# Optimization experiments

Measured on AMD Instinct MI355X. Metric: run time of the kernel, lower is better.

The kernel has to match this reference:

```python
import jax, jax.numpy as jnp
import numpy as np

B, C, H, W = 2, 1, 2048, 2048
RADIUS = 1
RK = 2 * RADIUS + 1  # 3
N = H * W
OBV_DECAY = 0.95


def setup_inputs() -> dict:
    key = jax.random.key(0)
    k1, k2, k3, k4, k5 = jax.random.split(key, 5)
    # x: [B, C+1, H, W]; channel 0 = spin field s, last channel = inverse temperature b (>0)
    x = jax.random.uniform(k1, (B, C + 1, H, W), dtype=jnp.float32)
    obvs = jax.random.uniform(k2, (B, 4, H, W), dtype=jnp.float32)
    # learned coupling table, center tap zeroed (no self-coupling)
    J = jax.random.uniform(k3, (1, RK * RK, N), dtype=jnp.float32)
    J = J.at[:, RADIUS * RK + RADIUS, :].set(0.0)
    # explicit RNG draws (torch.rand_like equivalents) for determinism
    rand_s = jax.random.uniform(k4, (B, C, H, W), dtype=jnp.float32)
    rand_drop = jax.random.uniform(k5, (1, 1, H, W), dtype=jnp.float32)
    return {"x": x, "obvs": obvs, "J": J, "rand_s": rand_s, "rand_drop": rand_drop}


def _unfold3(s):
    # F.unfold(circular_pad(s,1), 3) for a single-channel map: [B,1,H,W] -> [B,9,H*W]
    sp = jnp.pad(s, ((0, 0), (0, 0), (1, 1), (1, 1)), mode='wrap')
    patches = jnp.stack(
        [sp[:, 0, i:i + H, j:j + W] for i in range(RK) for j in range(RK)], axis=1
    )  # [B, 9, H, W], kernel positions row-major (matches F.unfold)
    return patches.reshape(s.shape[0], RK * RK, N)


def reference(x, obvs, J, rand_s, rand_drop):
    s = x[:, :C]          # [B,1,H,W] spins
    b = x[:, -1:]         # [B,1,H,W] inverse temperature
    sf = s.reshape(s.shape[0], 1, N)                 # unfold(s, 1)
    sJs = 2.0 * sf * (_unfold3(s) * J)               # [B,9,N]
    delta_e = sJs.sum(axis=1).reshape(s.shape)       # [B,1,H,W]
    E = -0.5 * delta_e

    # EMA observables
    e, e2, c, m = obvs[:, 0:1], obvs[:, 1:2], obvs[:, 2:3], obvs[:, 3:4]
    d = OBV_DECAY
    e = d * e + (1.0 - d) * E
    e2 = d * e2 + (1.0 - d) * E ** 2
    c = d * c + (1.0 - d) * (e2 - e ** 2) * b ** 2
    m = d * m + (1.0 - d) * s
    obvs_out = jnp.concatenate([e, e2, c, m], axis=1)  # [B,4,H,W]

    p = jnp.where(delta_e <= 0.0, jnp.ones_like(s), jnp.exp(-delta_e * b))
    accept = (rand_s < p) & (rand_drop > 0.5)
    flip = -2.0 * accept.astype(s.dtype) + 1.0

    state = jnp.concatenate([s * flip, b], axis=1)    # [B,2,H,W]
    return state, obvs_out
```

## Files before the change

kernel.cpp:

```cpp
#include <hip/hip_runtime.h>
#include <math.h>

namespace {
constexpr int H = 2048;
constexpr int W = 2048;
constexpr int NPIX = H * W;
constexpr int B = 2;
constexpr float DECf = 0.95f;
constexpr float OMDf = 1.0f - 0.95f;
}

using f4 = __attribute__((ext_vector_type(4))) float;

__global__ __launch_bounds__(256, 4) void ising_step_kernel(
    const float* __restrict__ x,
    const float* __restrict__ obvs,
    const float* __restrict__ Jm,
    const float* __restrict__ rs,
    const float* __restrict__ rd,
    float* __restrict__ out)
{
  const int bid = blockIdx.x;
  const int u   = ((bid & 7) << 10) | (bid >> 3);
  const int bi  = u >> 12;
  const int h   = (u >> 1) & (H - 1);
  const int w0  = ((u & 1) << 10) | (threadIdx.x << 2);
  const int n0  = (h << 11) | w0;

  const float* sbase = x + (size_t)bi * 2 * NPIX;
  const int hm = (h - 1) & (H - 1);
  const int hp = (h + 1) & (H - 1);
  const float* rowm = sbase + (size_t)hm * W;
  const float* rowc = sbase + (size_t)h  * W;
  const float* rowp = sbase + (size_t)hp * W;
  const int wl = (w0 - 1) & (W - 1);
  const int wr = (w0 + 4) & (W - 1);

  const f4 vm = *(const f4*)(rowm + w0);
  const f4 vc = *(const f4*)(rowc + w0);
  const f4 vp = *(const f4*)(rowp + w0);
  const float lm = rowm[wl], rm = rowm[wr];
  const float lc = rowc[wl], rc = rowc[wr];
  const float lp = rowp[wl], rp = rowp[wr];

  f4 jv[8];
  #pragma unroll
  for (int k = 0; k < 8; ++k) {
    const int kk = (k < 4) ? k : (k + 1);
    jv[k] = *(const f4*)(Jm + (size_t)kk * NPIX + n0);
  }

  const f4 bv  = *(const f4*)(sbase + (size_t)NPIX + n0);
  const float* ob = obvs + (size_t)bi * 4 * NPIX + n0;
  const f4 ev  = *(const f4*)(ob);
  const f4 e2v = *(const f4*)(ob + (size_t)NPIX);
  const f4 cv  = *(const f4*)(ob + 2 * (size_t)NPIX);
  const f4 mv  = *(const f4*)(ob + 3 * (size_t)NPIX);
  const f4 rv  = *(const f4*)(rs + (size_t)bi * NPIX + n0);
  const f4 dv  = *(const f4*)(rd + n0);

  const float am[6] = {lm, vm.x, vm.y, vm.z, vm.w, rm};
  const float ac[6] = {lc, vc.x, vc.y, vc.z, vc.w, rc};
  const float ap[6] = {lp, vp.x, vp.y, vp.z, vp.w, rp};

  const float bq[4]  = {bv.x, bv.y, bv.z, bv.w};
  const float eq[4]  = {ev.x, ev.y, ev.z, ev.w};
  const float e2q[4] = {e2v.x, e2v.y, e2v.z, e2v.w};
  const float cq[4]  = {cv.x, cv.y, cv.z, cv.w};
  const float mq[4]  = {mv.x, mv.y, mv.z, mv.w};
  const float rsq[4] = {rv.x, rv.y, rv.z, rv.w};
  const float rdq[4] = {dv.x, dv.y, dv.z, dv.w};

  float so[4], eo[4], e2o[4], co[4], mo[4];
  #pragma unroll
  for (int t = 0; t < 4; ++t) {
    const double sum =
        (double)jv[0][t] * am[t]     + (double)jv[1][t] * am[t + 1] +
        (double)jv[2][t] * am[t + 2] + (double)jv[3][t] * ac[t]     +
        (double)jv[4][t] * ac[t + 2] + (double)jv[5][t] * ap[t]     +
        (double)jv[6][t] * ap[t + 1] + (double)jv[7][t] * ap[t + 2];
    const float sf  = ac[t + 1];
    const double s  = (double)sf;
    const double de = 2.0 * s * sum;
    const double p  = (de <= 0.0) ? 1.0 : exp(-de * (double)bq[t]);
    const bool acc  = ((double)rsq[t] < p) && (rdq[t] > 0.5f);
    const float E   = (float)(-s * sum);
    const float bf  = bq[t];
    const float en  = DECf * eq[t]  + OMDf * E;
    const float e2n = DECf * e2q[t] + OMDf * E * E;
    const float cn  = DECf * cq[t]  + OMDf * (e2n - en * en) * bf * bf;
    const float mn  = DECf * mq[t]  + OMDf * sf;
    so[t]  = acc ? -sf : sf;
    eo[t]  = en;
    e2o[t] = e2n;
    co[t]  = cn;
    mo[t]  = mn;
  }

  float* st = out + (size_t)bi * 2 * NPIX;
  float* oo = out + (size_t)B * 2 * NPIX + (size_t)bi * 4 * NPIX;
  *(f4*)(st + n0)                     = (f4){so[0], so[1], so[2], so[3]};
  *(f4*)(st + (size_t)NPIX + n0)      = bv;
  *(f4*)(oo + n0)                     = (f4){eo[0], eo[1], eo[2], eo[3]};
  *(f4*)(oo + (size_t)NPIX + n0)      = (f4){e2o[0], e2o[1], e2o[2], e2o[3]};
  *(f4*)(oo + 2 * (size_t)NPIX + n0)  = (f4){co[0], co[1], co[2], co[3]};
  *(f4*)(oo + 3 * (size_t)NPIX + n0)  = (f4){mo[0], mo[1], mo[2], mo[3]};
}

extern "C" void kernel_launch(void* const* d_in, const int* in_sizes, int n_in,
                              void* d_out, int out_size, void* d_ws, size_t ws_size,
                              hipStream_t stream) {
  const float* x    = (const float*)d_in[0];
  const float* obvs = (const float*)d_in[1];
  const float* Jm   = (const float*)d_in[2];
  const float* rs   = (const float*)d_in[3];
  const float* rd   = (const float*)d_in[4];
  float* out = (float*)d_out;

  constexpr int grid = B * H * 2;
  ising_step_kernel<<<grid, 256, 0, stream>>>(x, obvs, Jm, rs, rd, out);
}
```

Baseline: 123.1 us.

## Process both batch elements per thread to reuse coupling and dropout loads

Each thread now computes both batch elements for its pixels, so the shared J coupling table and dropout mask are loaded once instead of once per batch. The grid is halved accordingly, the block-index swizzle is adjusted, and the occupancy hint is removed from launch bounds. This cuts global memory traffic for a bandwidth-bound kernel. In exchange it raises register pressure and per-thread latency exposure.

```diff
diff --git a/kernel.cpp b/kernel.cpp
--- a/kernel.cpp
+++ b/kernel.cpp
@@ -12,7 +12,7 @@
 
 using f4 = __attribute__((ext_vector_type(4))) float;
 
-__global__ __launch_bounds__(256, 4) void ising_step_kernel(
+__global__ __launch_bounds__(256) void ising_step_kernel(
     const float* __restrict__ x,
     const float* __restrict__ obvs,
     const float* __restrict__ Jm,
@@ -21,27 +21,15 @@
     float* __restrict__ out)
 {
   const int bid = blockIdx.x;
-  const int u   = ((bid & 7) << 10) | (bid >> 3);
-  const int bi  = u >> 12;
-  const int h   = (u >> 1) & (H - 1);
+  const int u   = ((bid & 7) << 9) | (bid >> 3);
+  const int h   = u >> 1;
   const int w0  = ((u & 1) << 10) | (threadIdx.x << 2);
   const int n0  = (h << 11) | w0;
 
-  const float* sbase = x + (size_t)bi * 2 * NPIX;
   const int hm = (h - 1) & (H - 1);
   const int hp = (h + 1) & (H - 1);
-  const float* rowm = sbase + (size_t)hm * W;
-  const float* rowc = sbase + (size_t)h  * W;
-  const float* rowp = sbase + (size_t)hp * W;
   const int wl = (w0 - 1) & (W - 1);
   const int wr = (w0 + 4) & (W - 1);
-
-  const f4 vm = *(const f4*)(rowm + w0);
-  const f4 vc = *(const f4*)(rowc + w0);
-  const f4 vp = *(const f4*)(rowp + w0);
-  const float lm = rowm[wl], rm = rowm[wr];
-  const float lc = rowc[wl], rc = rowc[wr];
-  const float lp = rowp[wl], rp = rowp[wr];
 
   f4 jv[8];
   #pragma unroll
@@ -49,62 +37,79 @@
     const int kk = (k < 4) ? k : (k + 1);
     jv[k] = *(const f4*)(Jm + (size_t)kk * NPIX + n0);
   }
+  const f4 dv = *(const f4*)(rd + n0);
 
-  const f4 bv  = *(const f4*)(sbase + (size_t)NPIX + n0);
-  const float* ob = obvs + (size_t)bi * 4 * NPIX + n0;
-  const f4 ev  = *(const f4*)(ob);
-  const f4 e2v = *(const f4*)(ob + (size_t)NPIX);
-  const f4 cv  = *(const f4*)(ob + 2 * (size_t)NPIX);
-  const f4 mv  = *(const f4*)(ob + 3 * (size_t)NPIX);
-  const f4 rv  = *(const f4*)(rs + (size_t)bi * NPIX + n0);
-  const f4 dv  = *(const f4*)(rd + n0);
-
-  const float am[6] = {lm, vm.x, vm.y, vm.z, vm.w, rm};
-  const float ac[6] = {lc, vc.x, vc.y, vc.z, vc.w, rc};
-  const float ap[6] = {lp, vp.x, vp.y, vp.z, vp.w, rp};
-
-  const float bq[4]  = {bv.x, bv.y, bv.z, bv.w};
-  const float eq[4]  = {ev.x, ev.y, ev.z, ev.w};
-  const float e2q[4] = {e2v.x, e2v.y, e2v.z, e2v.w};
-  const float cq[4]  = {cv.x, cv.y, cv.z, cv.w};
-  const float mq[4]  = {mv.x, mv.y, mv.z, mv.w};
-  const float rsq[4] = {rv.x, rv.y, rv.z, rv.w};
-  const float rdq[4] = {dv.x, dv.y, dv.z, dv.w};
-
-  float so[4], eo[4], e2o[4], co[4], mo[4];
+  f4 vm[2], vc[2], vp[2], bv[2], ev[2], e2v[2], cv[2], mv[2], rv[2];
+  float lm[2], rmh[2], lc[2], rch[2], lp[2], rph[2];
   #pragma unroll
-  for (int t = 0; t < 4; ++t) {
-    const double sum =
-        (double)jv[0][t] * am[t]     + (double)jv[1][t] * am[t + 1] +
-        (double)jv[2][t] * am[t + 2] + (double)jv[3][t] * ac[t]     +
-        (double)jv[4][t] * ac[t + 2] + (double)jv[5][t] * ap[t]     +
-        (double)jv[6][t] * ap[t + 1] + (double)jv[7][t] * ap[t + 2];
-    const float sf  = ac[t + 1];
-    const double s  = (double)sf;
-    const double de = 2.0 * s * sum;
-    const double p  = (de <= 0.0) ? 1.0 : exp(-de * (double)bq[t]);
-    const bool acc  = ((double)rsq[t] < p) && (rdq[t] > 0.5f);
-    const float E   = (float)(-s * sum);
-    const float bf  = bq[t];
-    const float en  = DECf * eq[t]  + OMDf * E;
-    const float e2n = DECf * e2q[t] + OMDf * E * E;
-    const float cn  = DECf * cq[t]  + OMDf * (e2n - en * en) * bf * bf;
-    const float mn  = DECf * mq[t]  + OMDf * sf;
-    so[t]  = acc ? -sf : sf;
-    eo[t]  = en;
-    e2o[t] = e2n;
-    co[t]  = cn;
-    mo[t]  = mn;
+  for (int bi = 0; bi < 2; ++bi) {
+    const float* sb   = x + (size_t)bi * 2 * NPIX;
+    const float* rowm = sb + (size_t)hm * W;
+    const float* rowc = sb + (size_t)h  * W;
+    const float* rowp = sb + (size_t)hp * W;
+    vm[bi] = *(const f4*)(rowm + w0);
+    vc[bi] = *(const f4*)(rowc + w0);
+    vp[bi] = *(const f4*)(rowp + w0);
+    lm[bi] = rowm[wl];  rmh[bi] = rowm[wr];
+    lc[bi] = rowc[wl];  rch[bi] = rowc[wr];
+    lp[bi] = rowp[wl];  rph[bi] = rowp[wr];
+    bv[bi] = *(const f4*)(sb + (size_t)NPIX + n0);
+    const float* ob = obvs + (size_t)bi * 4 * NPIX + n0;
+    ev[bi]  = *(const f4*)(ob);
+    e2v[bi] = *(const f4*)(ob + (size_t)NPIX);
+    cv[bi]  = *(const f4*)(ob + 2 * (size_t)NPIX);
+    mv[bi]  = *(const f4*)(ob + 3 * (size_t)NPIX);
+    rv[bi]  = *(const f4*)(rs + (size_t)bi * NPIX + n0);
   }
 
-  float* st = out + (size_t)bi * 2 * NPIX;
-  float* oo = out + (size_t)B * 2 * NPIX + (size_t)bi * 4 * NPIX;
-  *(f4*)(st + n0)                     = (f4){so[0], so[1], so[2], so[3]};
-  *(f4*)(st + (size_t)NPIX + n0)      = bv;
-  *(f4*)(oo + n0)                     = (f4){eo[0], eo[1], eo[2], eo[3]};
-  *(f4*)(oo + (size_t)NPIX + n0)      = (f4){e2o[0], e2o[1], e2o[2], e2o[3]};
-  *(f4*)(oo + 2 * (size_t)NPIX + n0)  = (f4){co[0], co[1], co[2], co[3]};
-  *(f4*)(oo + 3 * (size_t)NPIX + n0)  = (f4){mo[0], mo[1], mo[2], mo[3]};
+  #pragma unroll
+  for (int bi = 0; bi < 2; ++bi) {
+    const float am[6] = {lm[bi], vm[bi].x, vm[bi].y, vm[bi].z, vm[bi].w, rmh[bi]};
+    const float ac[6] = {lc[bi], vc[bi].x, vc[bi].y, vc[bi].z, vc[bi].w, rch[bi]};
+    const float ap[6] = {lp[bi], vp[bi].x, vp[bi].y, vp[bi].z, vp[bi].w, rph[bi]};
+    const float bq[4]  = {bv[bi].x, bv[bi].y, bv[bi].z, bv[bi].w};
+    const float eq[4]  = {ev[bi].x, ev[bi].y, ev[bi].z, ev[bi].w};
+    const float e2q[4] = {e2v[bi].x, e2v[bi].y, e2v[bi].z, e2v[bi].w};
+    const float cq[4]  = {cv[bi].x, cv[bi].y, cv[bi].z, cv[bi].w};
+    const float mq[4]  = {mv[bi].x, mv[bi].y, mv[bi].z, mv[bi].w};
+    const float rsq[4] = {rv[bi].x, rv[bi].y, rv[bi].z, rv[bi].w};
+    const float rdq[4] = {dv.x, dv.y, dv.z, dv.w};
+
+    float so[4], eo[4], e2o[4], co[4], mo[4];
+    #pragma unroll
+    for (int t = 0; t < 4; ++t) {
+      const double sum =
+          (double)jv[0][t] * am[t]     + (double)jv[1][t] * am[t + 1] +
+          (double)jv[2][t] * am[t + 2] + (double)jv[3][t] * ac[t]     +
+          (double)jv[4][t] * ac[t + 2] + (double)jv[5][t] * ap[t]     +
+          (double)jv[6][t] * ap[t + 1] + (double)jv[7][t] * ap[t + 2];
+      const float sf  = ac[t + 1];
+      const double s  = (double)sf;
+      const double de = 2.0 * s * sum;
+      const double p  = (de <= 0.0) ? 1.0 : exp(-de * (double)bq[t]);
+      const bool acc  = ((double)rsq[t] < p) && (rdq[t] > 0.5f);
+      const float E   = (float)(-s * sum);
+      const float bf  = bq[t];
+      const float en  = DECf * eq[t]  + OMDf * E;
+      const float e2n = DECf * e2q[t] + OMDf * E * E;
+      const float cn  = DECf * cq[t]  + OMDf * (e2n - en * en) * bf * bf;
+      const float mn  = DECf * mq[t]  + OMDf * sf;
+      so[t]  = acc ? -sf : sf;
+      eo[t]  = en;
+      e2o[t] = e2n;
+      co[t]  = cn;
+      mo[t]  = mn;
+    }
+
+    float* st = out + (size_t)bi * 2 * NPIX;
+    float* oo = out + (size_t)B * 2 * NPIX + (size_t)bi * 4 * NPIX;
+    *(f4*)(st + n0)                     = (f4){so[0], so[1], so[2], so[3]};
+    *(f4*)(st + (size_t)NPIX + n0)      = bv[bi];
+    *(f4*)(oo + n0)                     = (f4){eo[0], eo[1], eo[2], eo[3]};
+    *(f4*)(oo + (size_t)NPIX + n0)      = (f4){e2o[0], e2o[1], e2o[2], e2o[3]};
+    *(f4*)(oo + 2 * (size_t)NPIX + n0)  = (f4){co[0], co[1], co[2], co[3]};
+    *(f4*)(oo + 3 * (size_t)NPIX + n0)  = (f4){mo[0], mo[1], mo[2], mo[3]};
+  }
 }
 
 extern "C" void kernel_launch(void* const* d_in, const int* in_sizes, int n_in,
@@ -117,6 +122,6 @@
   const float* rd   = (const float*)d_in[4];
   float* out = (float*)d_out;
 
-  constexpr int grid = B * H * 2;
+  constexpr int grid = H * 2;
   ising_step_kernel<<<grid, 256, 0, stream>>>(x, obvs, Jm, rs, rd, out);
 }
```

After: 114.9 us. 1.07x faster.
